# Performance work log

Hardware: AMD Instinct MI355X
Metric: run time of the kernel (lower is better)

The kernel has to match this reference:

```python
import jax, jax.numpy as jnp
import numpy as np
from jax import lax


def _lstm_dir(x, W_ih, W_hh, b, reverse):
    # x: [B, T, D]; torch gate order i, f, g, o
    B, T, D = x.shape
    Hh = W_hh.shape[1]
    h0 = jnp.zeros((B, Hh), x.dtype)
    c0 = jnp.zeros((B, Hh), x.dtype)

    def step(carry, xt):
        h, c = carry
        g = xt @ W_ih.T + h @ W_hh.T + b
        i, f, gg, o = jnp.split(g, 4, axis=-1)
        c = jax.nn.sigmoid(f) * c + jax.nn.sigmoid(i) * jnp.tanh(gg)
        h = jax.nn.sigmoid(o) * jnp.tanh(c)
        return (h, c), h

    _, hs = lax.scan(step, (h0, c0), jnp.swapaxes(x, 0, 1), reverse=reverse)
    return jnp.swapaxes(hs, 0, 1)  # [B, T, Hh]


def _bilstm(x, w_ih_f, w_hh_f, b_f, w_ih_b, w_hh_b, b_b):
    fwd = _lstm_dir(x, w_ih_f, w_hh_f, b_f, reverse=False)
    bwd = _lstm_dir(x, w_ih_b, w_hh_b, b_b, reverse=True)
    return jnp.concatenate([fwd, bwd], axis=-1)


def setup_inputs() -> dict:
    key = jax.random.key(0)
    B, NS, L, H, LH, C = 8, 32, 128, 768, 256, 4
    ks = jax.random.split(key, 16)
    s = 0.05
    inp = {
        "hidden_states": jax.random.normal(ks[0], (B, NS, L, H), jnp.float32),
        "attention_mask": jax.random.randint(ks[1], (B, NS, L), 0, 2, jnp.int32),
        "wl_ih_f": jax.random.normal(ks[2], (4 * LH, H), jnp.float32) * s,
        "wl_hh_f": jax.random.normal(ks[3], (4 * LH, LH), jnp.float32) * s,
        "wl_b_f": jnp.zeros((4 * LH,), jnp.float32).at[LH:2 * LH].set(1.0),
        "wl_ih_b": jax.random.normal(ks[4], (4 * LH, H), jnp.float32) * s,
        "wl_hh_b": jax.random.normal(ks[5], (4 * LH, LH), jnp.float32) * s,
        "wl_b_b": jnp.zeros((4 * LH,), jnp.float32).at[LH:2 * LH].set(1.0),
        "ws_ih_f": jax.random.normal(ks[6], (4 * LH, 2 * LH), jnp.float32) * s,
        "ws_hh_f": jax.random.normal(ks[7], (4 * LH, LH), jnp.float32) * s,
        "ws_b_f": jnp.zeros((4 * LH,), jnp.float32).at[LH:2 * LH].set(1.0),
        "ws_ih_b": jax.random.normal(ks[8], (4 * LH, 2 * LH), jnp.float32) * s,
        "ws_hh_b": jax.random.normal(ks[9], (4 * LH, LH), jnp.float32) * s,
        "ws_b_b": jnp.zeros((4 * LH,), jnp.float32).at[LH:2 * LH].set(1.0),
        "cls_w": jax.random.uniform(ks[10], (C, 2 * LH), jnp.float32, -0.1, 0.1),
        "cls_b": jax.random.uniform(ks[11], (C,), jnp.float32, -0.1, 0.1),
    }
    return inp


def reference(hidden_states, attention_mask,
              wl_ih_f, wl_hh_f, wl_b_f, wl_ih_b, wl_hh_b, wl_b_b,
              ws_ih_f, ws_hh_f, ws_b_f, ws_ih_b, ws_hh_b, ws_b_b,
              cls_w, cls_b):
    B, NS, L, H = hidden_states.shape
    x = hidden_states.reshape(B * NS, L, H)
    m = attention_mask.reshape(B * NS, L).astype(x.dtype)

    # word-level bidirectional LSTM over each sentence
    h = _bilstm(x, wl_ih_f, wl_hh_f, wl_b_f, wl_ih_b, wl_hh_b, wl_b_b)  # [BN, L, 2LH]

    # per-sentence masked mean pooling (zeros for fully-masked sentences)
    cnt = m.sum(-1, keepdims=True)                    # [BN, 1]
    emb = jnp.einsum('btd,bt->bd', h, m) / jnp.maximum(cnt, 1.0)
    emb = jnp.where(cnt > 0, emb, 0.0)                # [BN, 2LH]
    emb = emb.reshape(B, NS, -1)

    # sentence-level bidirectional LSTM
    s = _bilstm(emb, ws_ih_f, ws_hh_f, ws_b_f, ws_ih_b, ws_hh_b, ws_b_b)  # [B, NS, 2LH]

    final = s[:, -1, :]  # dropout is identity in deterministic reference
    logits = final @ cls_w.T + cls_b
    return logits
```

## Files before the change

kernel.cpp:

```cpp
#include <hip/hip_runtime.h>
#include <math.h>


typedef __bf16 bf16x8 __attribute__((ext_vector_type(8)));
typedef float  f32x4  __attribute__((ext_vector_type(4)));

__device__ __forceinline__ float sigmoidf_(float x){ return 1.0f/(1.0f+expf(-x)); }
__device__ __forceinline__ unsigned short f2bf(float x){
    unsigned int b = __float_as_uint(x);
    b += 0x7FFFu + ((b>>16)&1u);
    return (unsigned short)(b>>16);
}
__device__ __forceinline__ float bf2f(unsigned short h){
    return __uint_as_float(((unsigned int)h)<<16);
}
__device__ __forceinline__ void split_bf(float x, unsigned short &hi, unsigned short &lo){
    hi = f2bf(x);
    lo = f2bf(x - bf2f(hi));
}
__device__ __forceinline__ uint4 pack8(const unsigned short* s){
    uint4 u;
    u.x = (unsigned)s[0] | ((unsigned)s[1]<<16);
    u.y = (unsigned)s[2] | ((unsigned)s[3]<<16);
    u.z = (unsigned)s[4] | ((unsigned)s[5]<<16);
    u.w = (unsigned)s[6] | ((unsigned)s[7]<<16);
    return u;
}

__device__ __forceinline__ void group_barrier(int* p, int members, int tid) {
    __syncthreads();
    if (tid == 0) {
        __hip_atomic_fetch_add(p, 1, __ATOMIC_RELAXED, __HIP_MEMORY_SCOPE_AGENT);
        int it = 0;
        while (__hip_atomic_load(p, __ATOMIC_RELAXED, __HIP_MEMORY_SCOPE_AGENT) < members) {
            __builtin_amdgcn_s_sleep(1);
            if (++it > (1<<22)) break;
        }
    }
    __builtin_amdgcn_fence(__ATOMIC_ACQUIRE, "workgroup");
    __syncthreads();
}

__device__ __forceinline__ unsigned tpat(int bid, int tid, int r) {
    unsigned v = (unsigned)bid * 1315423911u ^ (unsigned)tid * 2654435761u ^ 0x9E3779B9u;
    return r ? ~v : v;
}

__global__ void zero_f4(float4* __restrict__ p, int n) {
    int i = blockIdx.x * 256 + threadIdx.x;
    if (i < n) p[i] = make_float4(0.f, 0.f, 0.f, 0.f);
}

__global__ void prep_x(const float* __restrict__ X, unsigned short* __restrict__ Xsw) {
    int idx = blockIdx.x * 256 + threadIdx.x;
    int gblk = idx >> 6, ln = idx & 63;
    int mt = gblk / 24, kb = gblk - mt * 24;
    int m = mt * 16 + (ln & 15);
    int k = kb * 32 + (ln >> 4) * 8;
    const float* xp = X + (size_t)m * 768 + k;
    unsigned short hi[8], lo[8];
#pragma unroll
    for (int e = 0; e < 8; e += 4) {
        float4 v = *(const float4*)(xp + e);
        split_bf(v.x, hi[e+0], lo[e+0]);
        split_bf(v.y, hi[e+1], lo[e+1]);
        split_bf(v.z, hi[e+2], lo[e+2]);
        split_bf(v.w, hi[e+3], lo[e+3]);
    }
    *(uint4*)&Xsw[(size_t)gblk*1024 + ln*8]       = pack8(hi);
    *(uint4*)&Xsw[(size_t)gblk*1024 + 512 + ln*8] = pack8(lo);
}

__global__ void prep_wih_sw(const float* __restrict__ Wf, const float* __restrict__ Wb,
                            unsigned short* __restrict__ Wsw) {
    int idx = blockIdx.x * 256 + threadIdx.x;
    int gblk = idx >> 6, ln = idx & 63;
    int dir = gblk / 1536;
    int rem = gblk - dir * 1536;
    int ntile = rem / 24, kb = rem - ntile * 24;
    int j = ntile * 16 + (ln & 15);
    int k = kb * 32 + (ln >> 4) * 8;
    const float* wp = (dir ? Wb : Wf) + (size_t)j * 768 + k;
    unsigned short hi[8], lo[8];
#pragma unroll
    for (int e = 0; e < 8; e += 4) {
        float4 v = *(const float4*)(wp + e);
        split_bf(v.x, hi[e+0], lo[e+0]);
        split_bf(v.y, hi[e+1], lo[e+1]);
        split_bf(v.z, hi[e+2], lo[e+2]);
        split_bf(v.w, hi[e+3], lo[e+3]);
    }
    *(uint4*)&Wsw[(size_t)gblk*1024 + ln*8]       = pack8(hi);
    *(uint4*)&Wsw[(size_t)gblk*1024 + 512 + ln*8] = pack8(lo);
}

__global__ void prep_whh(const float* __restrict__ Wf, const float* __restrict__ Wb,
                         unsigned short* __restrict__ Wimg) {
    int idx = blockIdx.x * 256 + threadIdx.x;
    if (idx >= 524288) return;
    int dir = idx >> 18;
    int r   = idx & 262143;
    int u0t = r >> 14;
    int g   = (r >> 12) & 3;
    int u   = (r >> 8) & 15;
    int k   = r & 255;
    const float* W = dir ? Wb : Wf;
    float v = W[(size_t)(g*256 + u0t*16 + u) * 256 + k];
    unsigned short hi, lo; split_bf(v, hi, lo);
    size_t base = (size_t)(dir*16 + u0t) * 34816;
    Wimg[base + (g*16 + u)*264 + k]         = hi;
    Wimg[base + 16896 + (g*16 + u)*264 + k] = lo;
}

__global__ void transpose_whh(const float* __restrict__ Wf, const float* __restrict__ Wb,
                              float* __restrict__ Wt) {
    int idx = blockIdx.x * 256 + threadIdx.x;
    if (idx >= 524288) return;
    int dir = idx >> 18;
    int rem = idx & 262143;
    int k = rem >> 10;
    int j = rem & 1023;
    const float* Wp = dir ? Wb : Wf;
    Wt[idx] = Wp[j * 256 + k];
}

__global__ __launch_bounds__(256, 2) void proj_mfma(
    const unsigned short* __restrict__ Xsw,
    const unsigned short* __restrict__ Wihsw,
    const float* __restrict__ bfw, const float* __restrict__ bbw,
    float* __restrict__ Of, float* __restrict__ Ob)
{
    __shared__ unsigned short lds[24576];
    const int tid = threadIdx.x;
    const int d   = blockIdx.x + (blockIdx.y << 4);
    const int mt  = ((d & 7) << 4) | ((d >> 7) & 15);
    const int nt16 = (d >> 3) & 15;
    const int sel = nt16 >> 3;
    const int ntl = nt16 & 7;
    const float* bias = sel ? bbw : bfw;
    float* Op = sel ? Ob : Of;
    const int wv = tid >> 6, ln = tid & 63;
    const int c = ln & 15, q = ln >> 4;

    f32x4 acc[4][8];
#pragma unroll
    for (int i = 0; i < 4; i++)
#pragma unroll
        for (int j = 0; j < 8; j++) acc[i][j] = f32x4{0.f,0.f,0.f,0.f};

    const unsigned short* Abase = Xsw + (size_t)(mt*16) * 24 * 1024;
    const unsigned short* Bbase = Wihsw + (size_t)(sel*64 + ntl*8) * 24 * 1024;

#pragma unroll 1
    for (int kb = 0; kb < 24; kb++) {
        __syncthreads();
#pragma unroll
        for (int jj = 0; jj < 12; jj++) {
            int cc = wv + 4*jj;
            int isB = (cc >= 32);
            int blk = isB ? ((cc - 32) >> 1) : (cc >> 1);
            int half = cc & 1;
            const unsigned short* src = (isB ? Bbase : Abase)
                                        + (size_t)(blk*24 + kb)*1024 + half*512 + ln*8;
            unsigned short* dst = lds + (isB ? 16384 : 0) + blk*1024 + half*512 + ln*8;
            __builtin_amdgcn_global_load_lds(
                (const __attribute__((address_space(1))) unsigned int*)src,
                (__attribute__((address_space(3))) unsigned int*)dst, 16, 0, 0);
        }
        __syncthreads();

        bf16x8 bhv[8], blv[8];
#pragma unroll
        for (int cb = 0; cb < 8; cb++) {
            bhv[cb] = *(const bf16x8*)&lds[16384 + cb*1024 + ln*8];
            blv[cb] = *(const bf16x8*)&lds[16384 + cb*1024 + 512 + ln*8];
        }
#pragma unroll
        for (int rb = 0; rb < 4; rb++) {
            int it = wv*4 + rb;
            bf16x8 ah = *(const bf16x8*)&lds[it*1024 + ln*8];
            bf16x8 al = *(const bf16x8*)&lds[it*1024 + 512 + ln*8];
#pragma unroll
            for (int cb = 0; cb < 8; cb++) {
                acc[rb][cb] = __builtin_amdgcn_mfma_f32_16x16x32_bf16(ah, bhv[cb], acc[rb][cb], 0,0,0);
                acc[rb][cb] = __builtin_amdgcn_mfma_f32_16x16x32_bf16(ah, blv[cb], acc[rb][cb], 0,0,0);
                acc[rb][cb] = __builtin_amdgcn_mfma_f32_16x16x32_bf16(al, bhv[cb], acc[rb][cb], 0,0,0);
            }
        }
    }

#pragma unroll
    for (int rb = 0; rb < 4; rb++) {
        int mbase = mt*256 + (wv*4 + rb)*16 + q*4;
#pragma unroll
        for (int cb = 0; cb < 8; cb++) {
            int j = ntl*128 + cb*16 + c;
            float bv = bias[j];
#pragma unroll
            for (int reg = 0; reg < 4; reg++) {
                int m = mbase + reg;
                int tt = m & 127, nn = m >> 7;
                Op[(size_t)(tt*256 + nn)*1024 + j] = acc[rb][cb][reg] + bv;
            }
        }
    }
}

__global__ __launch_bounds__(256, 1) void word_recur(
    const float* __restrict__ Gf, const float* __restrict__ Gb,
    const unsigned short* __restrict__ Wimg,
    unsigned short* __restrict__ hA, unsigned short* __restrict__ hB,
    const int* __restrict__ mask,
    float* __restrict__ pooled, int* __restrict__ cnt,
    int* __restrict__ pf, unsigned int* __restrict__ tstg)
{
    extern __shared__ char ldsbuf[];
    unsigned short* Hl = (unsigned short*)ldsbuf;
    float* gex   = (float*)(ldsbuf + 36864);
    int*   mk_lds= (int*)(ldsbuf + 46080);

    const int tid = threadIdx.x;
    const int bid = blockIdx.x;
    const int dir = (bid >> 3) & 1;
    const int nt  = bid & 7;
    const int u0t = bid >> 4;
    const int grp = bid & 15;
    const float* G = dir ? Gb : Gf;

    const int wv = tid >> 6, ln = tid & 63;
    const int c = ln & 15, q = ln >> 4;

    int* mycnt = cnt + grp * 136;

    bool fast;
    {
        unsigned* tl = (unsigned*)ldsbuf;
        int* oks = (int*)(ldsbuf + 4096);
        int okl = 1;
#pragma unroll 1
        for (int r = 0; r < 2; r++) {
            __hip_atomic_store(&tstg[bid*256 + tid], tpat(bid, tid, r),
                               __ATOMIC_RELAXED, __HIP_MEMORY_SCOPE_AGENT);
            group_barrier(mycnt + 127 + 2*r, 16, tid);
            {
                int pbid = grp + 16*((u0t + 1 + wv) & 15);
                __builtin_amdgcn_global_load_lds(
                    (const __attribute__((address_space(1))) unsigned int*)
                        ((const char*)(tstg + pbid*256) + ln*16),
                    (__attribute__((address_space(3))) unsigned int*)(ldsbuf + wv*1024),
                    16, 0, 0x11 );
            }
            __syncthreads();
#pragma unroll
            for (int w2 = 0; w2 < 4; w2++) {
                int pb2 = grp + 16*((u0t + 1 + w2) & 15);
                okl &= (tl[w2*256 + tid] == tpat(pb2, tid, r)) ? 1 : 0;
            }
            group_barrier(mycnt + 128 + 2*r, 16, tid);
        }
        oks[tid] = okl;
        __syncthreads();
        if (tid == 0) {
            int o = 1;
            for (int i = 0; i < 256; i++) o &= oks[i];
            __hip_atomic_store(&pf[bid], o, __ATOMIC_RELAXED, __HIP_MEMORY_SCOPE_AGENT);
        }
        group_barrier(mycnt + 131, 16, tid);
        int f = 1;
#pragma unroll 1
        for (int k = 0; k < 16; k++)
            f &= __hip_atomic_load(&pf[grp + 16*k],
                                   __ATOMIC_RELAXED, __HIP_MEMORY_SCOPE_AGENT);
        fast = (f != 0);
    }

    {
        const char* msrc = (const char*)(mask + nt*32*128);
#pragma unroll
        for (int j = 0; j < 4; j++) {
            int i = wv + 4*j;
            __builtin_amdgcn_global_load_lds(
                (const __attribute__((address_space(1))) unsigned int*)(msrc + i*1024 + ln*16),
                (__attribute__((address_space(3))) unsigned int*)(((char*)mk_lds) + i*1024), 16, 0, 0);
        }
    }
    const unsigned short* wbase = Wimg + (size_t)(dir*16 + u0t) * 34816;
    bf16x8 wh_[8], wlo[8];
#pragma unroll
    for (int kb = 0; kb < 8; kb++) {
        wh_[kb] = *(const bf16x8*)&wbase[(wv*16 + c)*264 + kb*32 + q*8];
        wlo[kb] = *(const bf16x8*)&wbase[16896 + (wv*16 + c)*264 + kb*32 + q*8];
    }

    const int nl  = tid >> 3;
    const int up  = tid & 7;
    const int u0  = up*2;
    const int ug0 = u0t*16 + u0;
    const int n   = nt*32 + nl;

    float c0 = 0.f, c1 = 0.f, p0 = 0.f, p1 = 0.f;

    float2 gp[4];
    {
        const int te0 = dir ? 127 : 0;
        const float* Ga = G + (size_t)(te0*256 + n)*1024 + ug0;
#pragma unroll
        for (int g = 0; g < 4; g++) gp[g] = *(const float2*)&Ga[g*256];
    }

#pragma unroll 1
    for (int t = 0; t < 128; ++t) {
        const int te = dir ? (127 - t) : t;
        const unsigned short* hin = (t & 1) ? hB : hA;
        unsigned short* hout = ((t & 1) ? hA : hB) + (size_t)(dir*8 + nt) * 18432;

        if (fast) {
            const char* hsrc = (const char*)(hin + (size_t)(dir*8 + nt) * 18432);
#pragma unroll
            for (int j = 0; j < 9; j++) {
                int i = wv + 4*j;
                __builtin_amdgcn_global_load_lds(
                    (const __attribute__((address_space(1))) unsigned int*)(hsrc + i*1024 + ln*16),
                    (__attribute__((address_space(3))) unsigned int*)(ldsbuf + i*1024),
                    16, 0, 0x11 );
            }
        } else {
            const unsigned long long* hsrc =
                (const unsigned long long*)(hin + (size_t)(dir*8 + nt) * 18432);
            unsigned long long* hdst = (unsigned long long*)ldsbuf;
#pragma unroll
            for (int j = 0; j < 18; j++) {
                unsigned long long v = __hip_atomic_load(hsrc + tid + 256*j,
                        __ATOMIC_RELAXED, __HIP_MEMORY_SCOPE_AGENT);
                hdst[tid + 256*j] = v;
            }
        }
        __syncthreads();

        f32x4 acc[2];
        acc[0] = f32x4{0.f,0.f,0.f,0.f};
        acc[1] = f32x4{0.f,0.f,0.f,0.f};
#pragma unroll
        for (int kb = 0; kb < 8; kb++) {
#pragma unroll
            for (int sb = 0; sb < 2; sb++) {
                bf16x8 bh = *(const bf16x8*)&Hl[(sb*16 + c)*264 + kb*32 + q*8];
                bf16x8 bl = *(const bf16x8*)&Hl[8448 + (sb*16 + c)*264 + kb*32 + q*8];
                acc[sb] = __builtin_amdgcn_mfma_f32_16x16x32_bf16(wh_[kb], bh, acc[sb], 0, 0, 0);
                acc[sb] = __builtin_amdgcn_mfma_f32_16x16x32_bf16(wh_[kb], bl, acc[sb], 0, 0, 0);
                acc[sb] = __builtin_amdgcn_mfma_f32_16x16x32_bf16(wlo[kb], bh, acc[sb], 0, 0, 0);
            }
        }
#pragma unroll
        for (int sb = 0; sb < 2; sb++)
#pragma unroll
            for (int reg = 0; reg < 4; reg++)
                gex[(wv*16 + q*4 + reg)*36 + sb*16 + c] = acc[sb][reg];
        __syncthreads();

        float2 gpn[4];
        if (t < 127) {
            const int te1 = dir ? (126 - t) : (t + 1);
            const float* Ga = G + (size_t)(te1*256 + n)*1024 + ug0;
#pragma unroll
            for (int g = 0; g < 4; g++) gpn[g] = *(const float2*)&Ga[g*256];
        }

        const int mk = mk_lds[nl*128 + te];
        float iv0 = gex[(0*16 + u0)*36 + nl] + gp[0].x;
        float fv0 = gex[(1*16 + u0)*36 + nl] + gp[1].x;
        float gv0 = gex[(2*16 + u0)*36 + nl] + gp[2].x;
        float ov0 = gex[(3*16 + u0)*36 + nl] + gp[3].x;
        float iv1 = gex[(0*16 + u0+1)*36 + nl] + gp[0].y;
        float fv1 = gex[(1*16 + u0+1)*36 + nl] + gp[1].y;
        float gv1 = gex[(2*16 + u0+1)*36 + nl] + gp[2].y;
        float ov1 = gex[(3*16 + u0+1)*36 + nl] + gp[3].y;
        float cn0 = sigmoidf_(fv0)*c0 + sigmoidf_(iv0)*tanhf(gv0);
        float hn0 = sigmoidf_(ov0)*tanhf(cn0);
        float cn1 = sigmoidf_(fv1)*c1 + sigmoidf_(iv1)*tanhf(gv1);
        float hn1 = sigmoidf_(ov1)*tanhf(cn1);
        c0 = cn0; c1 = cn1;
        if (mk) { p0 += hn0; p1 += hn1; }
        if (t != 127) {
            unsigned short h0h, h0l, h1h, h1l;
            split_bf(hn0, h0h, h0l);
            split_bf(hn1, h1h, h1l);
            unsigned int dhi = (unsigned)h0h | ((unsigned)h1h << 16);
            unsigned int dlo = (unsigned)h0l | ((unsigned)h1l << 16);
            unsigned int* hw = (unsigned int*)hout;
            __hip_atomic_store(&hw[nl*132 + u0t*8 + up], dhi,
                               __ATOMIC_RELAXED, __HIP_MEMORY_SCOPE_AGENT);
            __hip_atomic_store(&hw[4224 + nl*132 + u0t*8 + up], dlo,
                               __ATOMIC_RELAXED, __HIP_MEMORY_SCOPE_AGENT);
        }

        if (t < 127) {
            group_barrier(mycnt + t, 16, tid);
#pragma unroll
            for (int g = 0; g < 4; g++) gp[g] = gpn[g];
        }
    }

    int cntN = 0;
#pragma unroll 1
    for (int te2 = 0; te2 < 128; ++te2) cntN += mk_lds[nl*128 + te2];
    float inv = 1.0f / fmaxf((float)cntN, 1.0f);
    *(float2*)&pooled[n*512 + dir*256 + ug0] = make_float2(p0*inv, p1*inv);
}

__global__ __launch_bounds__(256) void word_step_mfma(
    const float* __restrict__ Gf, const float* __restrict__ Gb,
    const unsigned short* __restrict__ Wimg,
    const unsigned short* __restrict__ hin_img,
    unsigned short* __restrict__ hout_img,
    const int* __restrict__ mask,
    float* __restrict__ c_st, float* __restrict__ pooled, int t)
{
    extern __shared__ char ldsbuf[];
    unsigned short* Wl = (unsigned short*)ldsbuf;
    unsigned short* Hl = Wl + 34816;
    float* gex = (float*)(ldsbuf + 69632 + 36864);

    const int tid = threadIdx.x;
    const int bid = blockIdx.x;
    const int dir = bid >> 7;
    const int u0t = (bid >> 3) & 15;
    const int nt  = bid & 7;
    const int te  = dir ? (127 - t) : t;
    const float* G = dir ? Gb : Gf;

    const int wv = tid >> 6, ln = tid & 63;
    const int c = ln & 15, q = ln >> 4;

    {
        const char* wsrc = (const char*)(Wimg + (size_t)(dir*16 + u0t) * 34816);
        const char* hsrc = (const char*)(hin_img + (size_t)(dir*8 + nt) * 18432);
        char* wdst = (char*)Wl;
        char* hdst = (char*)Hl;
#pragma unroll
        for (int j = 0; j < 17; j++) {
            int i = wv + 4*j;
            __builtin_amdgcn_global_load_lds(
                (const __attribute__((address_space(1))) unsigned int*)(wsrc + i*1024 + ln*16),
                (__attribute__((address_space(3))) unsigned int*)(wdst + i*1024), 16, 0, 0);
        }
#pragma unroll
        for (int j = 0; j < 9; j++) {
            int i = wv + 4*j;
            __builtin_amdgcn_global_load_lds(
                (const __attribute__((address_space(1))) unsigned int*)(hsrc + i*1024 + ln*16),
                (__attribute__((address_space(3))) unsigned int*)(hdst + i*1024), 16, 0, 0);
        }
    }

    const int uu = tid & 15;
    const int np = tid >> 4;
    const int uglob = u0t*16 + uu;
    const int n_a = nt*32 + np*2;
    float gpre[8]; int mk0, mk1; float cold0, cold1, pold0, pold1;
    {
        const float* Ga = G + (size_t)(te*256 + n_a)*1024 + uglob;
        const float* Gc = Ga + 1024;
#pragma unroll
        for (int g = 0; g < 4; g++) { gpre[g] = Ga[g*256]; gpre[4+g] = Gc[g*256]; }
        mk0 = mask[n_a*128 + te];
        mk1 = mask[(n_a + 1)*128 + te];
        cold0 = c_st[dir*65536 + n_a*256 + uglob];
        cold1 = c_st[dir*65536 + (n_a + 1)*256 + uglob];
        pold0 = pooled[n_a*512 + dir*256 + uglob];
        pold1 = pooled[(n_a + 1)*512 + dir*256 + uglob];
    }
    __syncthreads();

    f32x4 acc[2];
    acc[0] = f32x4{0.f,0.f,0.f,0.f};
    acc[1] = f32x4{0.f,0.f,0.f,0.f};
#pragma unroll
    for (int kb = 0; kb < 8; kb++) {
        bf16x8 ahh = *(const bf16x8*)&Wl[(wv*16 + c)*264 + kb*32 + q*8];
        bf16x8 all_ = *(const bf16x8*)&Wl[16896 + (wv*16 + c)*264 + kb*32 + q*8];
#pragma unroll
        for (int sb = 0; sb < 2; sb++) {
            bf16x8 bh = *(const bf16x8*)&Hl[(sb*16 + c)*264 + kb*32 + q*8];
            bf16x8 bl = *(const bf16x8*)&Hl[8448 + (sb*16 + c)*264 + kb*32 + q*8];
            acc[sb] = __builtin_amdgcn_mfma_f32_16x16x32_bf16(ahh, bh, acc[sb], 0, 0, 0);
            acc[sb] = __builtin_amdgcn_mfma_f32_16x16x32_bf16(ahh, bl, acc[sb], 0, 0, 0);
            acc[sb] = __builtin_amdgcn_mfma_f32_16x16x32_bf16(all_, bh, acc[sb], 0, 0, 0);
        }
    }
#pragma unroll
    for (int sb = 0; sb < 2; sb++)
#pragma unroll
        for (int reg = 0; reg < 4; reg++)
            gex[(wv*16 + q*4 + reg)*36 + sb*16 + c] = acc[sb][reg];
    __syncthreads();

    unsigned short* hout = hout_img + (size_t)(dir*8 + nt) * 18432;
    {
        int nl = np*2;
        float iv = gex[(0*16 + uu)*36 + nl] + gpre[0];
        float fv = gex[(1*16 + uu)*36 + nl] + gpre[1];
        float gv = gex[(2*16 + uu)*36 + nl] + gpre[2];
        float ov = gex[(3*16 + uu)*36 + nl] + gpre[3];
        float cn = sigmoidf_(fv)*cold0 + sigmoidf_(iv)*tanhf(gv);
        float hn = sigmoidf_(ov)*tanhf(cn);
        c_st[dir*65536 + n_a*256 + uglob] = cn;
        unsigned short hh, hl; split_bf(hn, hh, hl);
        hout[nl*264 + uglob] = hh;
        hout[8448 + nl*264 + uglob] = hl;
        if (mk0) pooled[n_a*512 + dir*256 + uglob] = pold0 + hn;
    }
    {
        int nl = np*2 + 1;
        float iv = gex[(0*16 + uu)*36 + nl] + gpre[4];
        float fv = gex[(1*16 + uu)*36 + nl] + gpre[5];
        float gv = gex[(2*16 + uu)*36 + nl] + gpre[6];
        float ov = gex[(3*16 + uu)*36 + nl] + gpre[7];
        float cn = sigmoidf_(fv)*cold1 + sigmoidf_(iv)*tanhf(gv);
        float hn = sigmoidf_(ov)*tanhf(cn);
        c_st[dir*65536 + (n_a+1)*256 + uglob] = cn;
        unsigned short hh, hl; split_bf(hn, hh, hl);
        hout[nl*264 + uglob] = hh;
        hout[8448 + nl*264 + uglob] = hl;
        if (mk1) pooled[(n_a+1)*512 + dir*256 + uglob] = pold1 + hn;
    }
}

__global__ __launch_bounds__(256) void gemm_proj(
    const float* __restrict__ A, int M, int K,
    const float* __restrict__ Wf, const float* __restrict__ Wb,
    const float* __restrict__ bf, const float* __restrict__ bb,
    float* __restrict__ Of, float* __restrict__ Ob)
{
    __shared__ float As[16][132];
    __shared__ float Bs[16][132];
    const int t = threadIdx.x;
    const int n0 = blockIdx.x * 128;
    const int m0 = blockIdx.y * 128;
    const int sel = (n0 >= 1024);
    const float* Wp = sel ? Wb : Wf;
    const float* bp = sel ? bb : bf;
    float* Op = sel ? Ob : Of;
    const int n0d = n0 & 1023;
    const int tm = t >> 4;
    const int tn = t & 15;

    float acc[8][8];
#pragma unroll
    for (int i = 0; i < 8; i++)
#pragma unroll
        for (int j = 0; j < 8; j++) acc[i][j] = 0.f;

    for (int k0 = 0; k0 < K; k0 += 16) {
        __syncthreads();
#pragma unroll
        for (int rr = 0; rr < 2; rr++) {
            int idx = t + rr * 256;
            int row = idx >> 2, kq = idx & 3;
            float4 v = *(const float4*)&A[(size_t)(m0 + row) * K + k0 + kq * 4];
            As[kq*4+0][row] = v.x; As[kq*4+1][row] = v.y;
            As[kq*4+2][row] = v.z; As[kq*4+3][row] = v.w;
        }
#pragma unroll
        for (int rr = 0; rr < 2; rr++) {
            int idx = t + rr * 256;
            int row = idx >> 2, kq = idx & 3;
            float4 v = *(const float4*)&Wp[(size_t)(n0d + row) * K + k0 + kq * 4];
            Bs[kq*4+0][row] = v.x; Bs[kq*4+1][row] = v.y;
            Bs[kq*4+2][row] = v.z; Bs[kq*4+3][row] = v.w;
        }
        __syncthreads();
#pragma unroll
        for (int k = 0; k < 16; k++) {
            float4 a0 = *(const float4*)&As[k][tm*4];
            float4 a1 = *(const float4*)&As[k][tm*4+64];
            float4 b0 = *(const float4*)&Bs[k][tn*4];
            float4 b1 = *(const float4*)&Bs[k][tn*4+64];
            float av[8] = {a0.x,a0.y,a0.z,a0.w,a1.x,a1.y,a1.z,a1.w};
            float bv[8] = {b0.x,b0.y,b0.z,b0.w,b1.x,b1.y,b1.z,b1.w};
#pragma unroll
            for (int i = 0; i < 8; i++)
#pragma unroll
                for (int j = 0; j < 8; j++)
                    acc[i][j] += av[i] * bv[j];
        }
    }

#pragma unroll
    for (int ih = 0; ih < 2; ih++) {
#pragma unroll
        for (int i = 0; i < 4; i++) {
            int m = m0 + ih*64 + tm*4 + i;
#pragma unroll
            for (int jh = 0; jh < 2; jh++) {
                int col = n0d + jh*64 + tn*4;
                float4 bias4 = *(const float4*)&bp[col];
                float4 r;
                r.x = acc[ih*4+i][jh*4+0] + bias4.x;
                r.y = acc[ih*4+i][jh*4+1] + bias4.y;
                r.z = acc[ih*4+i][jh*4+2] + bias4.z;
                r.w = acc[ih*4+i][jh*4+3] + bias4.w;
                *(float4*)&Op[(size_t)m * 1024 + col] = r;
            }
        }
    }
}

__global__ __launch_bounds__(256) void pool_div(float* __restrict__ pooled,
                                                const int* __restrict__ mask) {
    __shared__ float red[256];
    int n = blockIdx.x, t = threadIdx.x;
    red[t] = (t < 128) ? (float)mask[n*128 + t] : 0.f;
    __syncthreads();
    for (int off = 128; off > 0; off >>= 1) {
        if (t < off) red[t] += red[t + off];
        __syncthreads();
    }
    float inv = 1.0f / fmaxf(red[0], 1.0f);
    pooled[n*512 + t] *= inv;
    pooled[n*512 + 256 + t] *= inv;
}

__global__ __launch_bounds__(256) void sent_step(
    const float* __restrict__ Gsf, const float* __restrict__ Gsb,
    const float* __restrict__ Wt,
    const float* __restrict__ h_in, float* __restrict__ h_out,
    float* __restrict__ c_s, float* __restrict__ final_h, int s)
{
    __shared__ float h_lds[256];
    __shared__ float part[256];
    __shared__ float ex[4][33];
    const int tid = threadIdx.x;
    const int bx = blockIdx.x;
    const int dir = bx >> 6;
    const int rb = bx & 63;
    const int b = rb >> 3;
    const int ut = rb & 7;
    const int u0 = ut * 32;
    const int t_eff = dir ? (31 - s) : s;
    const float* Gs = dir ? Gsb : Gsf;

    if (tid < 64) {
        float4 v = *(const float4*)&h_in[dir*2048 + b*256 + tid*4];
        *(float4*)&h_lds[tid*4] = v;
    }
    __syncthreads();

    const int kh = tid >> 7;
    const int rr = tid & 127;
    const int g = rr >> 5;
    const int uu = rr & 31;
    const int j = g*256 + u0 + uu;
    const float* wp = Wt + dir*262144 + kh*128*1024 + j;
    float acc = 0.f;
#pragma unroll 8
    for (int k = 0; k < 128; k++)
        acc += wp[k*1024] * h_lds[kh*128 + k];
    part[tid] = acc;
    __syncthreads();
    if (tid < 128) ex[g][uu] = part[tid] + part[tid + 128];
    __syncthreads();

    if (tid < 32) {
        int u = u0 + tid;
        size_t gb = (size_t)(b*32 + t_eff)*1024 + u;
        float iv = ex[0][tid] + Gs[gb];
        float fv = ex[1][tid] + Gs[gb + 256];
        float gv = ex[2][tid] + Gs[gb + 512];
        float ov = ex[3][tid] + Gs[gb + 768];
        int ci = dir*2048 + b*256 + u;
        float cold = c_s[ci];
        float cn = sigmoidf_(fv)*cold + sigmoidf_(iv)*tanhf(gv);
        float hn = sigmoidf_(ov)*tanhf(cn);
        c_s[ci] = cn;
        h_out[ci] = hn;
        if (t_eff == 31) final_h[b*512 + dir*256 + u] = hn;
    }
}

__global__ __launch_bounds__(256) void logits_k(const float* __restrict__ fh,
                                                const float* __restrict__ cw,
                                                const float* __restrict__ cb,
                                                float* __restrict__ out) {
    __shared__ float red[256];
    int tid = threadIdx.x;
    int o = tid >> 3;
    int b = o >> 2; int c = o & 3;
    int pp = tid & 7;
    float acc = 0.f;
    const float* fv = fh + b*512 + pp*64;
    const float* wv = cw + c*512 + pp*64;
#pragma unroll 8
    for (int e = 0; e < 64; e++) acc += fv[e]*wv[e];
    red[tid] = acc;
    __syncthreads();
    if (pp == 0) {
        float s = 0.f;
#pragma unroll
        for (int qq = 0; qq < 8; qq++) s += red[o*8 + qq];
        out[o] = s + cb[c];
    }
}

extern "C" void kernel_launch(void* const* d_in, const int* in_sizes, int n_in,
                              void* d_out, int out_size, void* d_ws, size_t ws_size,
                              hipStream_t stream) {
    const float* X       = (const float*)d_in[0];
    const int*   mask    = (const int*)d_in[1];
    const float* wl_ih_f = (const float*)d_in[2];
    const float* wl_hh_f = (const float*)d_in[3];
    const float* wl_b_f  = (const float*)d_in[4];
    const float* wl_ih_b = (const float*)d_in[5];
    const float* wl_hh_b = (const float*)d_in[6];
    const float* wl_b_b  = (const float*)d_in[7];
    const float* ws_ih_f = (const float*)d_in[8];
    const float* ws_hh_f = (const float*)d_in[9];
    const float* ws_b_f  = (const float*)d_in[10];
    const float* ws_ih_b = (const float*)d_in[11];
    const float* ws_hh_b = (const float*)d_in[12];
    const float* ws_b_b  = (const float*)d_in[13];
    const float* cls_w   = (const float*)d_in[14];
    const float* cls_b   = (const float*)d_in[15];
    float* out = (float*)d_out;
    float* w = (float*)d_ws;
    (void)in_sizes; (void)n_in; (void)out_size; (void)ws_size;

    float* Gf     = w;
    float* Gb     = Gf + 33554432;
    float* Gsf    = Gb + 33554432;
    float* Gsb    = Gsf + 262144;
    float* Wt     = Gsb + 262144;
    int*   cnt_w  = (int*)Wt;
    int*   cnt_s  = cnt_w + 2176;
    int*   pf     = cnt_s + 640;
    unsigned int* tstg = (unsigned int*)(pf + 256);
    float* finalh = Wt + 524288;
    float* pooled = finalh + 4096;
    float* c_st   = pooled + 131072;
    float* hs0    = c_st + 131072;
    float* hs1    = hs0 + 4096;
    float* cs     = hs1 + 4096;
    unsigned short* hA = (unsigned short*)(cs + 4096);
    unsigned short* hB = hA + 294912;
    unsigned short* Xsw   = hB + 294912;
    unsigned short* Wihsw = Xsw + 50331648;
    unsigned short* Wimg  = Wihsw + 3145728;

    zero_f4<<<412, 256, 0, stream>>>((float4*)pooled, 105472);
    zero_f4<<<3, 256, 0, stream>>>((float4*)cnt_w, 704);
    prep_x<<<12288, 256, 0, stream>>>(X, Xsw);
    prep_wih_sw<<<768, 256, 0, stream>>>(wl_ih_f, wl_ih_b, Wihsw);
    prep_whh<<<2048, 256, 0, stream>>>(wl_hh_f, wl_hh_b, Wimg);

    proj_mfma<<<dim3(16, 128), 256, 0, stream>>>(Xsw, Wihsw, wl_b_f, wl_b_b, Gf, Gb);

    {
        (void)hipGetLastError();
        word_recur<<<256, 256, 62464, stream>>>(Gf, Gb, Wimg, hA, hB, mask,
                                                pooled, cnt_w, pf, tstg);
        hipError_t e = hipGetLastError();
        if (e != hipSuccess) {
            hipFuncSetAttribute((const void*)word_step_mfma,
                                hipFuncAttributeMaxDynamicSharedMemorySize, 115712);
            for (int t = 0; t < 128; t++) {
                const unsigned short* hin = (t & 1) ? hB : hA;
                unsigned short* hout      = (t & 1) ? hA : hB;
                word_step_mfma<<<256, 256, 115712, stream>>>(Gf, Gb, Wimg, hin, hout,
                                                             mask, c_st, pooled, t);
            }
            pool_div<<<256, 256, 0, stream>>>(pooled, mask);
        }
    }

    transpose_whh<<<2048, 256, 0, stream>>>(ws_hh_f, ws_hh_b, Wt);

    gemm_proj<<<dim3(16, 2), 256, 0, stream>>>(pooled, 256, 512,
                                               ws_ih_f, ws_ih_b, ws_b_f, ws_b_b,
                                               Gsf, Gsb);

    for (int s = 0; s < 32; s++) {
        float* hin  = (s & 1) ? hs1 : hs0;
        float* hout = (s & 1) ? hs0 : hs1;
        sent_step<<<128, 256, 0, stream>>>(Gsf, Gsb, Wt, hin, hout, cs, finalh, s);
    }

    logits_k<<<1, 256, 0, stream>>>(finalh, cls_w, cls_b, out);
}
```

Baseline: 1.045 ms.

## Fuse sentence LSTM forward into persistent MFMA kernel and shortcut backward to one step

Replaces the 32 per-step sentence-level launches with one persistent 16-block kernel that keeps split-bf16 recurrent weights in registers, runs the recurrence with MFMA, and synchronises blocks through global group barriers. Because only the last time step of the sentence output is used, the backward direction is reduced to a single LSTM step from zero state, computed by a tiny kernel. This removes launch overhead and 31 backward steps. In exchange it relies on cross-block spin barriers and adds a second recurrent-weight prep pass.

```diff
diff --git a/kernel.cpp b/kernel.cpp
--- a/kernel.cpp
+++ b/kernel.cpp
@@ -621,6 +621,180 @@
     pooled[n*512 + 256 + t] *= inv;
 }
 
+__global__ __launch_bounds__(256, 1) void sent_fwd_mfma(
+    const float* __restrict__ Gsf,
+    const unsigned short* __restrict__ WimgS,
+    unsigned short* __restrict__ hsA, unsigned short* __restrict__ hsB,
+    float* __restrict__ final_h, int* __restrict__ cnt,
+    int* __restrict__ pf, unsigned int* __restrict__ tstg)
+{
+    extern __shared__ char ldsbuf[];
+    unsigned short* Him = (unsigned short*)ldsbuf;
+    float* gex = (float*)(ldsbuf + 17408);
+
+    const int tid = threadIdx.x;
+    const int bid = blockIdx.x;
+    const int u0t = bid;
+    const int wv = tid >> 6, ln = tid & 63;
+    const int c = ln & 15, q = ln >> 4;
+
+    int* mycnt = cnt;
+
+    bool fast;
+    {
+        unsigned* tl = (unsigned*)ldsbuf;
+        int* oks = (int*)(ldsbuf + 4096);
+        int okl = 1;
+#pragma unroll 1
+        for (int r = 0; r < 2; r++) {
+            __hip_atomic_store(&tstg[bid*256 + tid], tpat(bid, tid, r) ^ 0xA5A5A5A5u,
+                               __ATOMIC_RELAXED, __HIP_MEMORY_SCOPE_AGENT);
+            group_barrier(mycnt + 31 + 2*r, 16, tid);
+            {
+                int pbid = (bid + 1 + wv) & 15;
+                __builtin_amdgcn_global_load_lds(
+                    (const __attribute__((address_space(1))) unsigned int*)
+                        ((const char*)(tstg + pbid*256) + ln*16),
+                    (__attribute__((address_space(3))) unsigned int*)(ldsbuf + wv*1024),
+                    16, 0, 0x11 );
+            }
+            __syncthreads();
+#pragma unroll
+            for (int w2 = 0; w2 < 4; w2++) {
+                int pb2 = (bid + 1 + w2) & 15;
+                okl &= (tl[w2*256 + tid] == (tpat(pb2, tid, r) ^ 0xA5A5A5A5u)) ? 1 : 0;
+            }
+            group_barrier(mycnt + 32 + 2*r, 16, tid);
+        }
+        oks[tid] = okl;
+        __syncthreads();
+        if (tid == 0) {
+            int o = 1;
+            for (int i = 0; i < 256; i++) o &= oks[i];
+            __hip_atomic_store(&pf[bid], o, __ATOMIC_RELAXED, __HIP_MEMORY_SCOPE_AGENT);
+        }
+        group_barrier(mycnt + 35, 16, tid);
+        int f = 1;
+#pragma unroll 1
+        for (int k = 0; k < 16; k++)
+            f &= __hip_atomic_load(&pf[k],
+                                   __ATOMIC_RELAXED, __HIP_MEMORY_SCOPE_AGENT);
+        fast = (f != 0);
+    }
+
+    const unsigned short* wbase = WimgS + (size_t)u0t * 34816;
+    bf16x8 wh_[8], wlo[8];
+#pragma unroll
+    for (int kb = 0; kb < 8; kb++) {
+        wh_[kb] = *(const bf16x8*)&wbase[(wv*16 + c)*264 + kb*32 + q*8];
+        wlo[kb] = *(const bf16x8*)&wbase[16896 + (wv*16 + c)*264 + kb*32 + q*8];
+    }
+
+    const int up  = tid & 7;
+    const int b   = tid >> 3;
+    const int u0l = up*2;
+    const int ug0 = u0t*16 + u0l;
+
+    float c0 = 0.f, c1 = 0.f;
+
+#pragma unroll 1
+    for (int t = 0; t < 32; ++t) {
+        const unsigned short* hin = (t & 1) ? hsB : hsA;
+        unsigned short* hout = (t & 1) ? hsA : hsB;
+
+        float2 gp[4];
+        if (tid < 64) {
+            const float* Ga = Gsf + (size_t)(b*32 + t)*1024 + ug0;
+#pragma unroll
+            for (int g = 0; g < 4; g++) gp[g] = *(const float2*)&Ga[g*256];
+        }
+
+        if (fast) {
+            const char* hsrc = (const char*)hin;
+#pragma unroll
+            for (int j = 0; j < 5; j++) {
+                int i = wv + 4*j;
+                if (i < 17)
+                    __builtin_amdgcn_global_load_lds(
+                        (const __attribute__((address_space(1))) unsigned int*)(hsrc + i*1024 + ln*16),
+                        (__attribute__((address_space(3))) unsigned int*)(ldsbuf + i*1024),
+                        16, 0, 0x11 );
+            }
+        } else {
+            const unsigned long long* hsrc = (const unsigned long long*)hin;
+            unsigned long long* hdst = (unsigned long long*)ldsbuf;
+#pragma unroll
+            for (int j = 0; j < 9; j++) {
+                int idx = tid + 256*j;
+                if (idx < 2176) {
+                    unsigned long long v = __hip_atomic_load(hsrc + idx,
+                            __ATOMIC_RELAXED, __HIP_MEMORY_SCOPE_AGENT);
+                    hdst[idx] = v;
+                }
+            }
+        }
+        __syncthreads();
+
+        f32x4 acc = f32x4{0.f,0.f,0.f,0.f};
+#pragma unroll
+        for (int kb = 0; kb < 8; kb++) {
+            bf16x8 bh = *(const bf16x8*)&Him[c*264 + kb*32 + q*8];
+            bf16x8 bl = *(const bf16x8*)&Him[4224 + c*264 + kb*32 + q*8];
+            acc = __builtin_amdgcn_mfma_f32_16x16x32_bf16(wh_[kb], bh, acc, 0, 0, 0);
+            acc = __builtin_amdgcn_mfma_f32_16x16x32_bf16(wh_[kb], bl, acc, 0, 0, 0);
+            acc = __builtin_amdgcn_mfma_f32_16x16x32_bf16(wlo[kb], bh, acc, 0, 0, 0);
+        }
+#pragma unroll
+        for (int reg = 0; reg < 4; reg++)
+            gex[(wv*16 + q*4 + reg)*20 + c] = acc[reg];
+        __syncthreads();
+
+        if (tid < 64) {
+            float iv0 = gex[(0*16 + u0l  )*20 + b] + gp[0].x;
+            float fv0 = gex[(1*16 + u0l  )*20 + b] + gp[1].x;
+            float gv0 = gex[(2*16 + u0l  )*20 + b] + gp[2].x;
+            float ov0 = gex[(3*16 + u0l  )*20 + b] + gp[3].x;
+            float iv1 = gex[(0*16 + u0l+1)*20 + b] + gp[0].y;
+            float fv1 = gex[(1*16 + u0l+1)*20 + b] + gp[1].y;
+            float gv1 = gex[(2*16 + u0l+1)*20 + b] + gp[2].y;
+            float ov1 = gex[(3*16 + u0l+1)*20 + b] + gp[3].y;
+            float cn0 = sigmoidf_(fv0)*c0 + sigmoidf_(iv0)*tanhf(gv0);
+            float hn0 = sigmoidf_(ov0)*tanhf(cn0);
+            float cn1 = sigmoidf_(fv1)*c1 + sigmoidf_(iv1)*tanhf(gv1);
+            float hn1 = sigmoidf_(ov1)*tanhf(cn1);
+            c0 = cn0; c1 = cn1;
+            if (t != 31) {
+                unsigned short h0h, h0l, h1h, h1l;
+                split_bf(hn0, h0h, h0l);
+                split_bf(hn1, h1h, h1l);
+                unsigned int dhi = (unsigned)h0h | ((unsigned)h1h << 16);
+                unsigned int dlo = (unsigned)h0l | ((unsigned)h1l << 16);
+                unsigned int* hw = (unsigned int*)hout;
+                __hip_atomic_store(&hw[b*132 + u0t*8 + up], dhi,
+                                   __ATOMIC_RELAXED, __HIP_MEMORY_SCOPE_AGENT);
+                __hip_atomic_store(&hw[2112 + b*132 + u0t*8 + up], dlo,
+                                   __ATOMIC_RELAXED, __HIP_MEMORY_SCOPE_AGENT);
+            } else {
+                *(float2*)&final_h[b*512 + ug0] = make_float2(hn0, hn1);
+            }
+        }
+
+        if (t < 31) group_barrier(mycnt + t, 16, tid);
+    }
+}
+
+__global__ __launch_bounds__(256) void sent_bwd1(const float* __restrict__ Gsb,
+                                                 float* __restrict__ final_h) {
+    int b = blockIdx.x;
+    int u = threadIdx.x;
+    const float* Gr = Gsb + (size_t)(b*32 + 31)*1024 + u;
+    float iv = Gr[0], fv2 = Gr[256], gv = Gr[512], ov = Gr[768];
+    (void)fv2;
+    float cn = sigmoidf_(iv)*tanhf(gv);
+    float hn = sigmoidf_(ov)*tanhf(cn);
+    final_h[b*512 + 256 + u] = hn;
+}
+
 __global__ __launch_bounds__(256) void sent_step(
     const float* __restrict__ Gsf, const float* __restrict__ Gsb,
     const float* __restrict__ Wt,
@@ -745,12 +919,17 @@
     unsigned short* Xsw   = hB + 294912;
     unsigned short* Wihsw = Xsw + 50331648;
     unsigned short* Wimg  = Wihsw + 3145728;
+    unsigned short* WimgS = Wimg + 1114112;
+    unsigned short* hsA   = (unsigned short*)(WimgS + 1114112);
+    unsigned short* hsB   = hsA + 8704;
 
     zero_f4<<<412, 256, 0, stream>>>((float4*)pooled, 105472);
     zero_f4<<<3, 256, 0, stream>>>((float4*)cnt_w, 704);
+    zero_f4<<<9, 256, 0, stream>>>((float4*)hsA, 2176);
     prep_x<<<12288, 256, 0, stream>>>(X, Xsw);
     prep_wih_sw<<<768, 256, 0, stream>>>(wl_ih_f, wl_ih_b, Wihsw);
     prep_whh<<<2048, 256, 0, stream>>>(wl_hh_f, wl_hh_b, Wimg);
+    prep_whh<<<2048, 256, 0, stream>>>(ws_hh_f, ws_hh_b, WimgS);
 
     proj_mfma<<<dim3(16, 128), 256, 0, stream>>>(Xsw, Wihsw, wl_b_f, wl_b_b, Gf, Gb);
 
@@ -772,16 +951,25 @@
         }
     }
 
-    transpose_whh<<<2048, 256, 0, stream>>>(ws_hh_f, ws_hh_b, Wt);
-
     gemm_proj<<<dim3(16, 2), 256, 0, stream>>>(pooled, 256, 512,
                                                ws_ih_f, ws_ih_b, ws_b_f, ws_b_b,
                                                Gsf, Gsb);
 
-    for (int s = 0; s < 32; s++) {
-        float* hin  = (s & 1) ? hs1 : hs0;
-        float* hout = (s & 1) ? hs0 : hs1;
-        sent_step<<<128, 256, 0, stream>>>(Gsf, Gsb, Wt, hin, hout, cs, finalh, s);
+    sent_bwd1<<<8, 256, 0, stream>>>(Gsb, finalh);
+
+    {
+        (void)hipGetLastError();
+        sent_fwd_mfma<<<16, 256, 22528, stream>>>(Gsf, WimgS, hsA, hsB,
+                                                  finalh, cnt_s, pf, tstg);
+        hipError_t e = hipGetLastError();
+        if (e != hipSuccess) {
+            transpose_whh<<<2048, 256, 0, stream>>>(ws_hh_f, ws_hh_b, Wt);
+            for (int s = 0; s < 32; s++) {
+                float* hin  = (s & 1) ? hs1 : hs0;
+                float* hout = (s & 1) ? hs0 : hs1;
+                sent_step<<<128, 256, 0, stream>>>(Gsf, Gsb, Wt, hin, hout, cs, finalh, s);
+            }
+        }
     }
 
     logits_k<<<1, 256, 0, stream>>>(finalh, cls_w, cls_b, out);
```

Result: faster. 943.7 us (-9.7%).
